# Kernel optimization log

Measured on AMD Instinct MI355X. Metric: run time of the kernel, lower is better.

Reference implementation:

```python
import jax, jax.numpy as jnp
import numpy as np

EPS = 1e-12  # tf.nn.l2_normalize epsilon


def _l2norm(x, axis):
    # tf.nn.l2_normalize: x / sqrt(max(sum(x^2), eps))
    return x * jax.lax.rsqrt(jnp.maximum(jnp.sum(x * x, axis=axis, keepdims=True), EPS))


def setup_inputs() -> dict:
    key = jax.random.key(0)
    k0, k1, k2, k3 = jax.random.split(key, 4)
    B, L, E, C, NG = 128, 1024, 300, 20, 55
    return {
        "x_emb": jax.random.normal(k0, (B, L, E), jnp.float32),
        "x_mask": jnp.ones((B, L), jnp.float32),            # mask_seq = tf.ones(...) in call()
        "W_class": jax.random.normal(k1, (B, C, E), jnp.float32),
        "conv_w": jax.random.normal(k2, (NG, C, C), jnp.float32) * 0.05,  # [width, in=C, out=C]
        "conv_b": jnp.zeros((C,), jnp.float32),
        "W_dis": jax.random.normal(k3, (C, E), jnp.float32) * 0.05,       # 20 per-class 0-layer discriminators
        "b_dis": jnp.zeros((C,), jnp.float32),
    }


def reference(x_emb, x_mask, W_class, conv_w, conv_b, W_dis, b_dis):
    # --- att_emb_ngram_encoder_cnn ---
    x0 = x_emb * x_mask[..., None]                       # b s e (masked word embeddings)
    xn = _l2norm(x0, 2)                                  # b s e
    wn = _l2norm(W_class, 2)                             # b c e (normalize over embed dim)
    G = jnp.einsum('bse,bce->bsc', xn, wn)               # cosine label-word attention, b s c
    # ngram conv smoothing over sequence, SAME padding, relu
    att = jax.lax.conv_general_dilated(
        G, conv_w, window_strides=(1,), padding='SAME',
        dimension_numbers=('NWC', 'WIO', 'NWC')) + conv_b  # b s c
    att = jax.nn.relu(att)
    # partial (masked) softmax over sequence dim
    ew = jnp.exp(att) * x_mask[..., None]                # b s c
    beta = ew / jnp.sum(ew, axis=1, keepdims=True)       # b s c
    # per-class attentive pooling of (unmasked) word embeddings: H_enc b e c
    H = jnp.einsum('bse,bsc->bec', x_emb, beta)
    # --- 20 per-class 0-layer discriminators (dropout is identity at inference) ---
    logits = jnp.einsum('bec,ce->bc', H, W_dis) + b_dis  # b c
    return logits
```

## Files before the change

### kernel.cpp

```cpp
#include <hip/hip_runtime.h>
#include <math.h>

#define B 128
#define L 1024
#define E 300
#define C 20

#define OFF_WNT 0
#define OFF_WDT 768000
#define OFF_SWC 774000
#define OFF_G   796400
#define OFF_D   3417840
#define OFF_S   6039280
#define OFF_T   6041840

__global__ __launch_bounds__(256) void prep_kernel(
    const float* __restrict__ Wc, const float* __restrict__ convw,
    const float* __restrict__ wdis,
    float* __restrict__ wnT, float* __restrict__ wdT,
    float* __restrict__ swc, float* __restrict__ ST)
{
  int t = threadIdx.x;
  int gid = blockIdx.x * 256 + t;

  if (gid < 2 * B * C) ST[gid] = 0.f;

  if (gid < 55 * C * C) {
    int w  = gid / (C * C);
    int r  = gid % (C * C);
    int ci = r / C, co = r % C;
    swc[(((size_t)ci * 4 + co / 5) * 14 + (w >> 2)) * 20 + (co % 5) * 4 + (w & 3)] = convw[gid];
  }
  if (gid < C * C) {
    int ci = gid / C, co = gid % C;
    swc[(((size_t)ci * 4 + co / 5) * 14 + 13) * 20 + (co % 5) * 4 + 3] = 0.f;
  }
  if (gid < 6000) {
    int og = gid / 1500, rem = gid % 1500;
    int kq = rem / 20, i = rem % 20;
    int co = og * 5 + i / 4, q = i & 3;
    wdT[gid] = wdis[(size_t)co * E + kq * 4 + q];
  }

  int row = blockIdx.x * 4 + (t >> 6);
  int ln  = t & 63;
  if (row < B * C) {
    int bb = row / C, c = row % C;
    const float* src = Wc + (size_t)row * E;
    float v[5];
    float ss = 0.f;
    #pragma unroll
    for (int k = 0; k < 5; ++k) {
      int e = ln + 64 * k;
      v[k] = (e < E) ? src[e] : 0.f;
      ss += v[k] * v[k];
    }
    #pragma unroll
    for (int off = 32; off; off >>= 1) ss += __shfl_xor(ss, off, 64);
    float r = rsqrtf(fmaxf(ss, 1e-12f));
    float* dst = wnT + ((size_t)bb * 4 + c / 5) * 1500;
    int cosub = (c % 5) * 4;
    #pragma unroll
    for (int k = 0; k < 5; ++k) {
      int e = ln + 64 * k;
      if (e < E) dst[(e >> 2) * 20 + cosub + (e & 3)] = v[k] * r;
    }
  }
}

__global__ __launch_bounds__(256, 8) void gemm_kernel(
    const float* __restrict__ x, const float* __restrict__ wnT,
    const float* __restrict__ wdT, float* __restrict__ Gt, float* __restrict__ Dt)
{
  __shared__ float xs[32 * 64];

  int t  = threadIdx.x;
  int ln = t & 63;
  int og = __builtin_amdgcn_readfirstlane(t >> 6);
  int b  = blockIdx.y;
  int s0 = blockIdx.x * 64;

  const float* wnbase = wnT + ((size_t)b * 4 + og) * 1500;
  const float* wdbase = wdT + (size_t)og * 1500;

  int col = t & 7;
  int r0  = (t >> 3) * 2;
  int sw  = r0 ^ (col * 4);
  const float* xcol = x + ((size_t)b * L + s0 + r0) * E + col * 4;

  float accG[5] = {0.f, 0.f, 0.f, 0.f, 0.f};
  float accD[5] = {0.f, 0.f, 0.f, 0.f, 0.f};
  float ssq = 0.f;

  {
    float4 f0 = *(const float4*)(xcol);
    float4 f1 = *(const float4*)(xcol + E);
    #pragma unroll
    for (int j = 0; j < 4; ++j)
      *(float2*)&xs[(col * 4 + j) * 64 + sw] =
          make_float2(((const float*)&f0)[j], ((const float*)&f1)[j]);
  }
  __syncthreads();

  for (int chunk = 0; chunk < 10; ++chunk) {
    float4 f0, f1;
    int krem_n = E - (chunk + 1) * 32; if (krem_n > 32) krem_n = 32;
    bool ld = (chunk < 9) && (col * 4 < krem_n);
    if (ld) {
      const float* p = xcol + (chunk + 1) * 32;
      f0 = *(const float4*)(p);
      f1 = *(const float4*)(p + E);
    }

    int krem = E - chunk * 32; if (krem > 32) krem = 32;
    int nq = krem >> 2;
    bool own_ssq = ((chunk & 3) == og);
    #pragma unroll
    for (int kq = 0; kq < 8; ++kq) {
      if (kq < nq) {
        const float* wn_p = wnbase + (chunk * 8 + kq) * 20;
        const float* wd_p = wdbase + (chunk * 8 + kq) * 20;
        float wG[20], wD[20];
        #pragma unroll
        for (int i = 0; i < 20; ++i) { wG[i] = wn_p[i]; wD[i] = wd_p[i]; }
        const float* xr = &xs[kq * 4 * 64 + (ln ^ (kq * 4))];
        float xv[4];
        #pragma unroll
        for (int q = 0; q < 4; ++q) xv[q] = xr[q * 64];
        if (own_ssq) {
          #pragma unroll
          for (int q = 0; q < 4; ++q) ssq = fmaf(xv[q], xv[q], ssq);
        }
        #pragma unroll
        for (int q = 0; q < 4; ++q) {
          #pragma unroll
          for (int c = 0; c < 5; ++c) {
            accG[c] = fmaf(xv[q], wG[c * 4 + q], accG[c]);
            accD[c] = fmaf(xv[q], wD[c * 4 + q], accD[c]);
          }
        }
      }
    }
    __syncthreads();

    if (ld) {
      #pragma unroll
      for (int j = 0; j < 4; ++j)
        *(float2*)&xs[(col * 4 + j) * 64 + sw] =
            make_float2(((const float*)&f0)[j], ((const float*)&f1)[j]);
    }
    __syncthreads();
  }

  xs[og * 64 + ln] = ssq;
  __syncthreads();
  float rinv = rsqrtf(fmaxf(xs[ln] + xs[64 + ln] + xs[128 + ln] + xs[192 + ln],
                            1e-12f));

  int s = s0 + ln;
  #pragma unroll
  for (int c = 0; c < 5; ++c) {
    Gt[((size_t)b * C + og * 5 + c) * L + s] = accG[c] * rinv;
    Dt[((size_t)b * C + og * 5 + c) * L + s] = accD[c];
  }
}

#define GP 312
__global__ __launch_bounds__(512, 4) void conv_kernel(
    const float* __restrict__ Gt, const float* __restrict__ Dt,
    const float* __restrict__ swc, const float* __restrict__ convb,
    float* __restrict__ S, float* __restrict__ T)
{
  __shared__ float g_lds[C * GP];

  int t  = threadIdx.x;
  int ln = t & 63;
  int wid = __builtin_amdgcn_readfirstlane(t >> 6);
  int og  = wid & 3;
  int cih = wid >> 2;
  int b  = blockIdx.y;
  int s0 = blockIdx.x * 256;

  for (int c = 0; c < C; ++c)
    for (int h = t; h < GP; h += 512) {
      int s = s0 - 27 + h;
      g_lds[c * GP + h] = (s >= 0 && s < L) ? Gt[((size_t)b * C + c) * L + s] : 0.f;
    }
  __syncthreads();

  float acc[4][5];
  #pragma unroll
  for (int j = 0; j < 4; ++j)
    #pragma unroll
    for (int c = 0; c < 5; ++c) acc[j][c] = 0.f;

  for (int ci = cih * 10; ci < cih * 10 + 10; ++ci) {
    const float* gl = &g_lds[ci * GP + ln * 4];
    const float* wp = swc + ((size_t)ci * 4 + og) * 280;
    float4 g0 = *(const float4*)gl;
    #pragma unroll
    for (int wq = 0; wq < 14; ++wq) {
      float4 g1 = *(const float4*)(gl + wq * 4 + 4);
      float w[20];
      #pragma unroll
      for (int i = 0; i < 20; ++i) w[i] = wp[wq * 20 + i];
      float ga[7] = {g0.x, g0.y, g0.z, g0.w, g1.x, g1.y, g1.z};
      #pragma unroll
      for (int q = 0; q < 4; ++q) {
        #pragma unroll
        for (int j = 0; j < 4; ++j) {
          float gv = ga[q + j];
          #pragma unroll
          for (int c = 0; c < 5; ++c)
            acc[j][c] = fmaf(gv, w[c * 4 + q], acc[j][c]);
        }
      }
      g0 = g1;
    }
  }

  __syncthreads();
  float* scr = g_lds;
  int pr = (og * 64 + ln) * 21;
  if (cih == 1) {
    #pragma unroll
    for (int j = 0; j < 4; ++j)
      #pragma unroll
      for (int c = 0; c < 5; ++c) scr[pr + j * 5 + c] = acc[j][c];
  }
  __syncthreads();

  if (cih == 0) {
    #pragma unroll
    for (int j = 0; j < 4; ++j)
      #pragma unroll
      for (int c = 0; c < 5; ++c) acc[j][c] += scr[pr + j * 5 + c];

    float se[5], st_[5];
    int s = s0 + ln * 4;
    #pragma unroll
    for (int c = 0; c < 5; ++c) {
      float cb = convb[og * 5 + c];
      float4 d4 = *(const float4*)&Dt[((size_t)b * C + og * 5 + c) * L + s];
      const float* df = (const float*)&d4;
      float e0 = 0.f, e1 = 0.f;
      #pragma unroll
      for (int j = 0; j < 4; ++j) {
        float a = acc[j][c] + cb;
        float e = expf(fmaxf(a, 0.f));
        e0 += e;
        e1 += e * df[j];
      }
      se[c] = e0; st_[c] = e1;
    }
    #pragma unroll
    for (int c = 0; c < 5; ++c) {
      #pragma unroll
      for (int off = 32; off; off >>= 1) {
        se[c]  += __shfl_xor(se[c],  off, 64);
        st_[c] += __shfl_xor(st_[c], off, 64);
      }
    }
    if (ln == 0) {
      #pragma unroll
      for (int c = 0; c < 5; ++c) {
        atomicAdd(&S[b * C + og * 5 + c], se[c]);
        atomicAdd(&T[b * C + og * 5 + c], st_[c]);
      }
    }
  }
}

__global__ __launch_bounds__(256) void fin_kernel(
    const float* __restrict__ S, const float* __restrict__ T,
    const float* __restrict__ bdis, float* __restrict__ out)
{
  int i = blockIdx.x * 256 + threadIdx.x;
  if (i < B * C) out[i] = T[i] / S[i] + bdis[i % C];
}

extern "C" void kernel_launch(void* const* d_in, const int* in_sizes, int n_in,
                              void* d_out, int out_size, void* d_ws, size_t ws_size,
                              hipStream_t stream) {
  const float* x_emb = (const float*)d_in[0];
  const float* Wc    = (const float*)d_in[2];
  const float* convw = (const float*)d_in[3];
  const float* convb = (const float*)d_in[4];
  const float* wdis  = (const float*)d_in[5];
  const float* bdis  = (const float*)d_in[6];

  float* ws  = (float*)d_ws;
  float* wnT = ws + OFF_WNT;
  float* wdT = ws + OFF_WDT;
  float* swc = ws + OFF_SWC;
  float* Gt  = ws + OFF_G;
  float* Dt  = ws + OFF_D;
  float* S   = ws + OFF_S;
  float* T   = ws + OFF_T;
  float* out = (float*)d_out;

  prep_kernel<<<640, 256, 0, stream>>>(Wc, convw, wdis, wnT, wdT, swc, S);
  gemm_kernel<<<dim3(L / 64, B), 256, 0, stream>>>(x_emb, wnT, wdT, Gt, Dt);
  conv_kernel<<<dim3(L / 256, B), 512, 0, stream>>>(Gt, Dt, swc, convb, S, T);
  fin_kernel<<<10, 256, 0, stream>>>(S, T, bdis, out);
}
```

Baseline: 350.2 us.

## Replace LDS-staged gemm with direct vector loads and split-K shuffle reduction

The gemm kernel drops its shared-memory transpose staging and double-buffer syncs. Each 64-lane wave now handles 16 sequence rows, with 4 lanes per row splitting the embedding dimension. Each lane loads float4 chunks of x straight from global memory, and the partial sums are combined with lane shuffles. The grid grows fourfold, and each wave re-reads x for its own output group, so x traffic through L2 rises fourfold. This removes LDS traffic and barriers in exchange for more cache traffic and more scalar or vector weight loads.

```diff
diff --git a/kernel.cpp b/kernel.cpp
--- a/kernel.cpp
+++ b/kernel.cpp
@@ -72,96 +72,96 @@
     const float* __restrict__ x, const float* __restrict__ wnT,
     const float* __restrict__ wdT, float* __restrict__ Gt, float* __restrict__ Dt)
 {
-  __shared__ float xs[32 * 64];
-
   int t  = threadIdx.x;
   int ln = t & 63;
   int og = __builtin_amdgcn_readfirstlane(t >> 6);
   int b  = blockIdx.y;
-  int s0 = blockIdx.x * 64;
-
-  const float* wnbase = wnT + ((size_t)b * 4 + og) * 1500;
-  const float* wdbase = wdT + (size_t)og * 1500;
-
-  int col = t & 7;
-  int r0  = (t >> 3) * 2;
-  int sw  = r0 ^ (col * 4);
-  const float* xcol = x + ((size_t)b * L + s0 + r0) * E + col * 4;
+  int s0 = blockIdx.x * 16;
+  int qi = ln & 3;
+  int sr = ln >> 2;
+
+  const float* xrow = x   + ((size_t)b * L + s0 + sr) * E;
+  const float* wnb  = wnT + ((size_t)b * 4 + og) * 1500;
+  const float* wdb  = wdT + (size_t)og * 1500;
 
   float accG[5] = {0.f, 0.f, 0.f, 0.f, 0.f};
   float accD[5] = {0.f, 0.f, 0.f, 0.f, 0.f};
   float ssq = 0.f;
 
-  {
-    float4 f0 = *(const float4*)(xcol);
-    float4 f1 = *(const float4*)(xcol + E);
-    #pragma unroll
-    for (int j = 0; j < 4; ++j)
-      *(float2*)&xs[(col * 4 + j) * 64 + sw] =
-          make_float2(((const float*)&f0)[j], ((const float*)&f1)[j]);
-  }
-  __syncthreads();
-
-  for (int chunk = 0; chunk < 10; ++chunk) {
-    float4 f0, f1;
-    int krem_n = E - (chunk + 1) * 32; if (krem_n > 32) krem_n = 32;
-    bool ld = (chunk < 9) && (col * 4 < krem_n);
-    if (ld) {
-      const float* p = xcol + (chunk + 1) * 32;
-      f0 = *(const float4*)(p);
-      f1 = *(const float4*)(p + E);
-    }
-
-    int krem = E - chunk * 32; if (krem > 32) krem = 32;
-    int nq = krem >> 2;
-    bool own_ssq = ((chunk & 3) == og);
-    #pragma unroll
-    for (int kq = 0; kq < 8; ++kq) {
-      if (kq < nq) {
-        const float* wn_p = wnbase + (chunk * 8 + kq) * 20;
-        const float* wd_p = wdbase + (chunk * 8 + kq) * 20;
-        float wG[20], wD[20];
-        #pragma unroll
-        for (int i = 0; i < 20; ++i) { wG[i] = wn_p[i]; wD[i] = wd_p[i]; }
-        const float* xr = &xs[kq * 4 * 64 + (ln ^ (kq * 4))];
-        float xv[4];
-        #pragma unroll
-        for (int q = 0; q < 4; ++q) xv[q] = xr[q * 64];
-        if (own_ssq) {
-          #pragma unroll
-          for (int q = 0; q < 4; ++q) ssq = fmaf(xv[q], xv[q], ssq);
-        }
-        #pragma unroll
-        for (int q = 0; q < 4; ++q) {
-          #pragma unroll
-          for (int c = 0; c < 5; ++c) {
-            accG[c] = fmaf(xv[q], wG[c * 4 + q], accG[c]);
-            accD[c] = fmaf(xv[q], wD[c * 4 + q], accD[c]);
-          }
-        }
-      }
-    }
-    __syncthreads();
-
-    if (ld) {
-      #pragma unroll
-      for (int j = 0; j < 4; ++j)
-        *(float2*)&xs[(col * 4 + j) * 64 + sw] =
-            make_float2(((const float*)&f0)[j], ((const float*)&f1)[j]);
-    }
-    __syncthreads();
-  }
-
-  xs[og * 64 + ln] = ssq;
-  __syncthreads();
-  float rinv = rsqrtf(fmaxf(xs[ln] + xs[64 + ln] + xs[128 + ln] + xs[192 + ln],
-                            1e-12f));
-
-  int s = s0 + ln;
+  #pragma unroll 2
+  for (int tt = 0; tt < 9; ++tt) {
+    #pragma unroll
+    for (int sub = 0; sub < 2; ++sub) {
+      int kq = tt * 8 + qi * 2 + sub;
+      float4 xv = *(const float4*)(xrow + kq * 4);
+      const float4* wn4 = (const float4*)(wnb + kq * 20);
+      const float4* wd4 = (const float4*)(wdb + kq * 20);
+      ssq = fmaf(xv.x, xv.x, fmaf(xv.y, xv.y,
+            fmaf(xv.z, xv.z, fmaf(xv.w, xv.w, ssq))));
+      #pragma unroll
+      for (int c = 0; c < 5; ++c) {
+        float4 wg = wn4[c];
+        accG[c] = fmaf(xv.x, wg.x, accG[c]);
+        accG[c] = fmaf(xv.y, wg.y, accG[c]);
+        accG[c] = fmaf(xv.z, wg.z, accG[c]);
+        accG[c] = fmaf(xv.w, wg.w, accG[c]);
+      }
+      #pragma unroll
+      for (int c = 0; c < 5; ++c) {
+        float4 wv = wd4[c];
+        accD[c] = fmaf(xv.x, wv.x, accD[c]);
+        accD[c] = fmaf(xv.y, wv.y, accD[c]);
+        accD[c] = fmaf(xv.z, wv.z, accD[c]);
+        accD[c] = fmaf(xv.w, wv.w, accD[c]);
+      }
+    }
+  }
+  #pragma unroll
+  for (int sub = 0; sub < 2; ++sub) {
+    int kq = 72 + qi * 2 + sub;
+    if (kq < 75) {
+      float4 xv = *(const float4*)(xrow + kq * 4);
+      const float4* wn4 = (const float4*)(wnb + kq * 20);
+      const float4* wd4 = (const float4*)(wdb + kq * 20);
+      ssq = fmaf(xv.x, xv.x, fmaf(xv.y, xv.y,
+            fmaf(xv.z, xv.z, fmaf(xv.w, xv.w, ssq))));
+      #pragma unroll
+      for (int c = 0; c < 5; ++c) {
+        float4 wg = wn4[c];
+        accG[c] = fmaf(xv.x, wg.x, accG[c]);
+        accG[c] = fmaf(xv.y, wg.y, accG[c]);
+        accG[c] = fmaf(xv.z, wg.z, accG[c]);
+        accG[c] = fmaf(xv.w, wg.w, accG[c]);
+      }
+      #pragma unroll
+      for (int c = 0; c < 5; ++c) {
+        float4 wv = wd4[c];
+        accD[c] = fmaf(xv.x, wv.x, accD[c]);
+        accD[c] = fmaf(xv.y, wv.y, accD[c]);
+        accD[c] = fmaf(xv.z, wv.z, accD[c]);
+        accD[c] = fmaf(xv.w, wv.w, accD[c]);
+      }
+    }
+  }
+
   #pragma unroll
   for (int c = 0; c < 5; ++c) {
-    Gt[((size_t)b * C + og * 5 + c) * L + s] = accG[c] * rinv;
-    Dt[((size_t)b * C + og * 5 + c) * L + s] = accD[c];
+    accG[c] += __shfl_xor(accG[c], 1, 64);
+    accG[c] += __shfl_xor(accG[c], 2, 64);
+    accD[c] += __shfl_xor(accD[c], 1, 64);
+    accD[c] += __shfl_xor(accD[c], 2, 64);
+  }
+  ssq += __shfl_xor(ssq, 1, 64);
+  ssq += __shfl_xor(ssq, 2, 64);
+
+  if (qi == 0) {
+    float rinv = rsqrtf(fmaxf(ssq, 1e-12f));
+    int s = s0 + sr;
+    #pragma unroll
+    for (int c = 0; c < 5; ++c) {
+      Gt[((size_t)b * C + og * 5 + c) * L + s] = accG[c] * rinv;
+      Dt[((size_t)b * C + og * 5 + c) * L + s] = accD[c];
+    }
   }
 }
 
@@ -300,7 +300,7 @@
   float* out = (float*)d_out;
 
   prep_kernel<<<640, 256, 0, stream>>>(Wc, convw, wdis, wnT, wdT, swc, S);
-  gemm_kernel<<<dim3(L / 64, B), 256, 0, stream>>>(x_emb, wnT, wdT, Gt, Dt);
+  gemm_kernel<<<dim3(L / 16, B), 256, 0, stream>>>(x_emb, wnT, wdT, Gt, Dt);
   conv_kernel<<<dim3(L / 256, B), 512, 0, stream>>>(Gt, Dt, swc, convb, S, T);
   fin_kernel<<<10, 256, 0, stream>>>(S, T, bdis, out);
 }
```

Result: slower. 743.4 us (+112.3%).
